# Kernel optimization log

Hardware: AMD Instinct MI355X
Metric: run time of the kernel (lower is better)

Reference implementation:

```python
import jax, jax.numpy as jnp
import numpy as np

N, H, E, R, Q = 10000, 128, 160000, 32, 1
CUT = 5.0  # cutoff_upper, cutoff_lower = 0


def setup_inputs() -> dict:
    key = jax.random.key(0)
    ks = jax.random.split(key, 16)

    def w(k, shape, fan_in):
        return jax.random.normal(k, shape, jnp.float32) / np.sqrt(fan_in).astype(np.float32)

    return dict(
        X=jax.random.normal(ks[0], (N, H, 3, 3), jnp.float32),
        charges=jax.random.normal(ks[1], (N, Q), jnp.float32),
        edge_attr=jax.random.normal(ks[2], (E, R), jnp.float32),
        edge_weight=jax.random.uniform(ks[3], (E,), jnp.float32, 0.0, CUT),
        W1=w(ks[4], (H, R + 2 * Q), R + 2 * Q), b1=jnp.zeros((H,), jnp.float32),
        W2=w(ks[5], (2 * H, H), H), b2=jnp.zeros((2 * H,), jnp.float32),
        W3=w(ks[6], (3 * H, 2 * H), 2 * H), b3=jnp.zeros((3 * H,), jnp.float32),
        Wt0=w(ks[7], (H, H), H), Wt1=w(ks[8], (H, H), H), Wt2=w(ks[9], (H, H), H),
        Wt3=w(ks[10], (H, H), H), Wt4=w(ks[11], (H, H), H), Wt5=w(ks[12], (H, H), H),
        edge_index=jax.random.randint(ks[13], (2, E), 0, N),
    )


def tensor_norm(T):
    return jnp.sum(T * T, axis=(-2, -1))  # [N, H]


def decompose(T):
    # I: mean of diagonal (scalar per channel); A: skew part; S: traceless symmetric part
    I = jnp.trace(T, axis1=-2, axis2=-1) / 3.0  # [N, H]
    Tt = jnp.swapaxes(T, -2, -1)
    A = 0.5 * (T - Tt)
    S = 0.5 * (T + Tt) - I[..., None, None] * jnp.eye(3, dtype=T.dtype)
    return I, A, S


def chlin(T, W):
    # channel-mixing linear on [N, H, 3, 3]; torch Linear: y_o = sum_h x_h W[o, h]
    return jnp.einsum('nhij,oh->noij', T, W)


def vec_to_skew(v):
    # v: [N, H, 3] -> skew-symmetric [N, H, 3, 3]
    z = jnp.zeros_like(v[..., 0])
    return jnp.stack([
        jnp.stack([z, -v[..., 2], v[..., 1]], -1),
        jnp.stack([v[..., 2], z, -v[..., 0]], -1),
        jnp.stack([-v[..., 1], v[..., 0], z], -1),
    ], -2)


def skew_to_vec(A):
    return jnp.stack([A[..., 2, 1], A[..., 0, 2], A[..., 1, 0]], -1)


def reference(X, charges, edge_attr, edge_weight, W1, b1, W2, b2, W3, b3,
              Wt0, Wt1, Wt2, Wt3, Wt4, Wt5, edge_index):
    eye = jnp.eye(3, dtype=X.dtype)
    src, dst = edge_index[0], edge_index[1]
    n = X.shape[0]

    # cosine cutoff (cutoff_lower = 0)
    C = 0.5 * (jnp.cos(jnp.pi * edge_weight / CUT) + 1.0) * (edge_weight < CUT)

    # edge scalar MLP
    x = jnp.concatenate([edge_attr, charges[src], charges[dst]], axis=-1)
    x = jax.nn.silu(x @ W1.T + b1)
    x = jax.nn.silu(x @ W2.T + b2)
    x = jax.nn.silu(x @ W3.T + b3)
    x = (x * C[:, None]).reshape(-1, 3, H)  # [E, 3, H]

    X = X / (tensor_norm(X) + 1.0)[..., None, None]
    I, A, S = decompose(X)
    I = I @ Wt0.T
    A = chlin(A, Wt1)
    S = chlin(S, Wt2)
    Y = A + S + I[..., None, None] * eye

    # message passing: gather at dst, weight by edge scalars, scatter-add to src
    Im = jax.ops.segment_sum(x[:, 0, :] * I[dst], src, num_segments=n)
    Am = jax.ops.segment_sum(x[:, 1, :, None] * skew_to_vec(A)[dst], src, num_segments=n)
    Sm = jax.ops.segment_sum(x[:, 2, :, None, None] * S[dst], src, num_segments=n)
    msg = vec_to_skew(Am) + Sm + Im[..., None, None] * eye

    # O(3) equivariance: symmetrized product
    M = jnp.matmul(msg, Y) + jnp.matmul(Y, msg)
    I, A, S = decompose(M)

    _X = A + S + I[..., None, None] * eye
    normp1 = tensor_norm(_X) + 1.0
    I = I / normp1
    A = A / normp1[..., None, None]
    S = S / normp1[..., None, None]
    I = I @ Wt3.T
    A = chlin(A, Wt4)
    S = chlin(S, Wt5)
    dX = A + S + I[..., None, None] * eye
    return X + dX + jnp.matmul(dX, dX)
```

## Files before the change

### kernel.cpp

```cpp
#include <hip/hip_runtime.h>

#define NN  10000
#define HD  128
#define EE  160000
#define RD  32
#define NH  (NN * HD)

typedef __attribute__((ext_vector_type(8))) short short8_t;
typedef __attribute__((ext_vector_type(4))) float f32x4_t;
typedef __attribute__((ext_vector_type(4))) int   int4_t;

__device__ __forceinline__ float silu_f(float z) {
    return z * __builtin_amdgcn_rcpf(1.0f + __expf(-z));
}
__device__ __forceinline__ short f2b(float v) {
    unsigned u = __float_as_uint(v);
    unsigned r = (u + 0x7FFFu + ((u >> 16) & 1u)) >> 16;
    return (short)r;
}
__device__ __forceinline__ float b2f(short s) {
    return __uint_as_float(((unsigned)(unsigned short)s) << 16);
}
__device__ __forceinline__ unsigned cvt_pk(float a, float b) {
    unsigned r;
    asm("v_cvt_pk_bf16_f32 %0, %1, %2" : "=v"(r) : "v"(a), "v"(b));
    return r;
}

__global__ __launch_bounds__(256) void k_wconv(
    const float* __restrict__ W1, const float* __restrict__ W2,
    const float* __restrict__ W3,
    const float* __restrict__ Wt0, const float* __restrict__ Wt1,
    const float* __restrict__ Wt2, const float* __restrict__ Wt3,
    const float* __restrict__ Wt4, const float* __restrict__ Wt5,
    short* __restrict__ W1b, short* __restrict__ W2b, short* __restrict__ W3b,
    short* __restrict__ WtPh, short* __restrict__ WtPl,
    short* __restrict__ WtFh, short* __restrict__ WtFl)
{
    const int i = blockIdx.x * 256 + threadIdx.x;
    if (i < 8192) {
        const int j = i & 7, lane = (i >> 3) & 63;
        const int kb = (i >> 9) & 1, ct = i >> 10;
        const int n = ct * 16 + (lane & 15);
        const int k = kb * 32 + (lane >> 4) * 8 + j;
        W1b[i] = (k < 34) ? f2b(W1[n * 34 + k]) : (short)0;
        return;
    }
    int j2 = i - 8192;
    if (j2 < 32768) {
        const int j = j2 & 7, lane = (j2 >> 3) & 63;
        const int kb = (j2 >> 9) & 3, ct = j2 >> 11;
        const int n = ct * 16 + (lane & 15);
        const int k = kb * 32 + (lane >> 4) * 8 + j;
        W2b[j2] = f2b(W2[n * 128 + k]);
        return;
    }
    j2 -= 32768;
    if (j2 < 98304) {
        const int j = j2 & 7, lane = (j2 >> 3) & 63;
        const int kb = (j2 >> 9) & 7, ct = j2 >> 12;
        const int n = ct * 16 + (lane & 15);
        const int k = kb * 32 + (lane >> 4) * 8 + j;
        W3b[j2] = f2b(W3[n * 256 + k]);
        return;
    }
    j2 -= 98304;
    if (j2 < 6 * 16384) {
        const int m = j2 >> 14, idx = j2 & 16383;
        const float* src = (m == 0) ? Wt0 : (m == 1) ? Wt1 : (m == 2) ? Wt2
                         : (m == 3) ? Wt3 : (m == 4) ? Wt4 : Wt5;
        const float w = src[idx];
        const short hi = f2b(w);
        const short lo = f2b(w - b2f(hi));
        if (m < 3) { WtPh[m * 16384 + idx] = hi; WtPl[m * 16384 + idx] = lo; }
        else       { WtFh[(m - 3) * 16384 + idx] = hi; WtFl[(m - 3) * 16384 + idx] = lo; }
    }
}

template <bool FIN, bool WB>
__global__ __launch_bounds__(512, 4) void k_mix(
    const float* __restrict__ X,
    const float* __restrict__ Yin, const float* __restrict__ MSGin,
    const short* __restrict__ Wh,  const short* __restrict__ Wl,
    float* __restrict__ outp, short* __restrict__ ybf)
{
    extern __shared__ __align__(16) char smem[];
    short* sBh = (short*)smem;
    short* sBl = sBh + 144 * 128;
    float* sC  = (float*)smem;

    const int tid = threadIdx.x;
    const int n0  = blockIdx.x * 16;

#pragma unroll 2
    for (int i = 0; i < 4; i++) {
        const int p  = i * 512 + tid;
        const int nl = p >> 7, h = p & 127;
        float dec[9];
        if constexpr (!FIN) {
            const float* t = X + ((size_t)((n0 + nl) * HD + h)) * 9;
            float T[9];
#pragma unroll
            for (int q = 0; q < 9; q++) T[q] = t[q];
            float nrm = 0.f;
#pragma unroll
            for (int q = 0; q < 9; q++) nrm = fmaf(T[q], T[q], nrm);
            const float inv = 1.0f / (nrm + 1.0f);
#pragma unroll
            for (int q = 0; q < 9; q++) T[q] *= inv;
            const float I = (T[0] + T[4] + T[8]) * (1.0f / 3.0f);
            dec[0] = I;
            dec[1] = 0.5f * (T[7] - T[5]);
            dec[2] = 0.5f * (T[2] - T[6]);
            dec[3] = 0.5f * (T[3] - T[1]);
            dec[4] = T[0] - I;
            dec[5] = 0.5f * (T[1] + T[3]);
            dec[6] = 0.5f * (T[2] + T[6]);
            dec[7] = T[4] - I;
            dec[8] = 0.5f * (T[5] + T[7]);
        } else {
            const int basep = (n0 + nl) * HD + h;
            float yv[9], mv[9];
#pragma unroll
            for (int c = 0; c < 9; c++) {
                yv[c] = Yin[(size_t)c * NH + basep];
                mv[c] = MSGin[(size_t)c * NH + basep];
            }
            float Yt[9], G[9];
            {
                const float I = yv[0], a0 = yv[1], a1 = yv[2], a2 = yv[3];
                const float s00 = yv[4], s01 = yv[5], s02 = yv[6], s11 = yv[7], s12 = yv[8];
                const float s22 = -s00 - s11;
                Yt[0] = I + s00; Yt[1] = s01 - a2; Yt[2] = s02 + a1;
                Yt[3] = s01 + a2; Yt[4] = I + s11; Yt[5] = s12 - a0;
                Yt[6] = s02 - a1; Yt[7] = s12 + a0; Yt[8] = I + s22;
            }
            {
                const float I = mv[0], a0 = mv[1], a1 = mv[2], a2 = mv[3];
                const float s00 = mv[4], s01 = mv[5], s02 = mv[6], s11 = mv[7], s12 = mv[8];
                const float s22 = -s00 - s11;
                G[0] = I + s00; G[1] = s01 - a2; G[2] = s02 + a1;
                G[3] = s01 + a2; G[4] = I + s11; G[5] = s12 - a0;
                G[6] = s02 - a1; G[7] = s12 + a0; G[8] = I + s22;
            }
            float M[9];
#pragma unroll
            for (int r = 0; r < 3; r++)
#pragma unroll
                for (int cc = 0; cc < 3; cc++) {
                    float a = 0.f;
#pragma unroll
                    for (int k = 0; k < 3; k++)
                        a += G[r * 3 + k] * Yt[k * 3 + cc]
                           + Yt[r * 3 + k] * G[k * 3 + cc];
                    M[r * 3 + cc] = a;
                }
            const float I2 = (M[0] + M[4] + M[8]) * (1.0f / 3.0f);
            const float a0 = 0.5f * (M[7] - M[5]);
            const float a1 = 0.5f * (M[2] - M[6]);
            const float a2 = 0.5f * (M[3] - M[1]);
            const float s00 = M[0] - I2, s11 = M[4] - I2;
            const float s01 = 0.5f * (M[1] + M[3]);
            const float s02 = 0.5f * (M[2] + M[6]);
            const float s12 = 0.5f * (M[5] + M[7]);
            const float s22 = -s00 - s11;
            const float nrm = 2.f * (a0 * a0 + a1 * a1 + a2 * a2)
                            + (s00 * s00 + s11 * s11 + s22 * s22)
                            + 2.f * (s01 * s01 + s02 * s02 + s12 * s12)
                            + 3.f * I2 * I2;
            const float inv = 1.0f / (nrm + 1.0f);
            dec[0] = I2 * inv;  dec[1] = a0 * inv;  dec[2] = a1 * inv;
            dec[3] = a2 * inv;  dec[4] = s00 * inv; dec[5] = s01 * inv;
            dec[6] = s02 * inv; dec[7] = s11 * inv; dec[8] = s12 * inv;
        }
        const int sw = (nl & 7) << 3;
        const int hx = h ^ sw;
#pragma unroll
        for (int c = 0; c < 9; c++) {
            const float v  = dec[c];
            const short hi = f2b(v);
            const short lo = f2b(v - b2f(hi));
            const int idx = (c * 16 + nl) * 128 + hx;
            sBh[idx] = hi;
            sBl[idx] = lo;
        }
    }
    __syncthreads();

    const int lane = tid & 63, wid = tid >> 6;
    const int l15 = lane & 15, g = lane >> 4;
    f32x4_t acc[9];
#pragma unroll
    for (int c = 0; c < 9; c++) acc[c] = {0.f, 0.f, 0.f, 0.f};

    const int bsw = (l15 & 7) << 3;
    const int o   = wid * 16 + l15;
#pragma unroll
    for (int k = 0; k < 4; k++) {
        const int k0  = k * 32 + g * 8;
        const int ksw = k0 ^ bsw;
#pragma unroll
        for (int w = 0; w < 3; w++) {
            const size_t aoff = (size_t)w * 16384 + (size_t)o * 128 + k0;
            const short8_t Ah = *(const short8_t*)(Wh + aoff);
            const short8_t Al = *(const short8_t*)(Wl + aoff);
            const int ct0 = (w == 0) ? 0 : (w == 1 ? 1 : 4);
            const int ctn = (w == 0) ? 1 : (w == 1 ? 3 : 5);
            for (int cc = 0; cc < ctn; cc++) {
                const int ct = ct0 + cc;
                const int boff = (ct * 16 + l15) * 128 + ksw;
                const short8_t Bh = *(const short8_t*)&sBh[boff];
                const short8_t Bl = *(const short8_t*)&sBl[boff];
                acc[ct] = __builtin_amdgcn_mfma_f32_16x16x32_bf16(Al, Bh, acc[ct], 0, 0, 0);
                acc[ct] = __builtin_amdgcn_mfma_f32_16x16x32_bf16(Ah, Bl, acc[ct], 0, 0, 0);
                acc[ct] = __builtin_amdgcn_mfma_f32_16x16x32_bf16(Ah, Bh, acc[ct], 0, 0, 0);
            }
        }
    }
    __syncthreads();

    const int csw = (l15 & 7) << 2;
    {
        const int o0 = wid * 16 + g * 4;
#pragma unroll
        for (int ct = 0; ct < 9; ct++)
            *(f32x4_t*)&sC[(ct * 16 + l15) * 128 + (o0 ^ csw)] = acc[ct];
    }
    __syncthreads();

    if constexpr (!FIN) {
        for (int i = tid; i < 144 * 32; i += 512) {
            const int row = i >> 5, q = i & 31;
            const int c = row >> 4, nl = row & 15;
            const int sw = (nl & 7) << 2;
            const f32x4_t v = *(const f32x4_t*)&sC[row * 128 + ((q * 4) ^ sw)];
            const size_t oo = (size_t)c * NH + (size_t)(n0 + nl) * HD + q * 4;
            *(f32x4_t*)&outp[oo] = v;
            if constexpr (WB) {
                uint2 u;
                u.x = cvt_pk(v[0], v[1]);
                u.y = cvt_pk(v[2], v[3]);
                *(uint2*)&ybf[oo] = u;
            }
        }
    } else {
#pragma unroll 2
        for (int i = 0; i < 4; i++) {
            const int p  = i * 512 + tid;
            const int nl = p >> 7, oo = p & 127;
            const int sw = (nl & 7) << 2;
            const int ox = oo ^ sw;
            float a9[9];
#pragma unroll
            for (int c = 0; c < 9; c++) a9[c] = sC[(c * 16 + nl) * 128 + ox];
            float D[9];
            {
                const float I = a9[0], a0 = a9[1], a1 = a9[2], a2 = a9[3];
                const float s00 = a9[4], s01 = a9[5], s02 = a9[6];
                const float s11 = a9[7], s12 = a9[8];
                const float s22 = -s00 - s11;
                D[0] = I + s00; D[1] = s01 - a2; D[2] = s02 + a1;
                D[3] = s01 + a2; D[4] = I + s11; D[5] = s12 - a0;
                D[6] = s02 - a1; D[7] = s12 + a0; D[8] = I + s22;
            }
            const size_t xbase = ((size_t)((n0 + nl) * HD + oo)) * 9;
            float T[9];
#pragma unroll
            for (int q = 0; q < 9; q++) T[q] = X[xbase + q];
            float nrm = 0.f;
#pragma unroll
            for (int q = 0; q < 9; q++) nrm = fmaf(T[q], T[q], nrm);
            const float inv = 1.0f / (nrm + 1.0f);
            float* op = outp + xbase;
#pragma unroll
            for (int r = 0; r < 3; r++)
#pragma unroll
                for (int cc = 0; cc < 3; cc++) {
                    float dd2 = 0.f;
#pragma unroll
                    for (int k = 0; k < 3; k++)
                        dd2 = fmaf(D[r * 3 + k], D[k * 3 + cc], dd2);
                    op[r * 3 + cc] = T[r * 3 + cc] * inv + D[r * 3 + cc] + dd2;
                }
        }
    }
}

__global__ __launch_bounds__(256) void k_count(const int* __restrict__ EI,
                                               int* __restrict__ cnt)
{
    const int e = blockIdx.x * 256 + threadIdx.x;
    atomicAdd(&cnt[EI[e]], 1);
}

__global__ __launch_bounds__(256) void k_scan(const int* __restrict__ cnt,
                                              int* __restrict__ offs,
                                              int* __restrict__ cur)
{
    __shared__ int part[256];
    const int tid = threadIdx.x;
    const int per = (NN + 255) / 256;
    int s = 0;
    for (int i = 0; i < per; i++) {
        const int idx = tid * per + i;
        if (idx < NN) s += cnt[idx];
    }
    part[tid] = s;
    __syncthreads();
    if (tid == 0) {
        int r = 0;
        for (int i = 0; i < 256; i++) { const int t = part[i]; part[i] = r; r += t; }
        offs[NN] = r;
    }
    __syncthreads();
    int run = part[tid];
    for (int i = 0; i < per; i++) {
        const int idx = tid * per + i;
        if (idx < NN) {
            offs[idx] = run;
            cur[idx]  = run;
            run += cnt[idx];
        }
    }
}

__global__ __launch_bounds__(256) void k_fill(const int* __restrict__ EI,
                                              int* __restrict__ cur,
                                              int* __restrict__ EIDS,
                                              int* __restrict__ DSTS)
{
    const int e = blockIdx.x * 256 + threadIdx.x;
    const int s = EI[e];
    const int pos = atomicAdd(&cur[s], 1);
    EIDS[pos] = e;
    DSTS[pos] = EI[EE + e];
}

__global__ __launch_bounds__(512, 4) void k_edge_mfma(
    const float* __restrict__ EA, const float* __restrict__ CH,
    const float* __restrict__ EW, const int*   __restrict__ EI,
    const short* __restrict__ W1b, const float* __restrict__ b1,
    const short* __restrict__ W2b, const float* __restrict__ b2,
    const short* __restrict__ W3b, const float* __restrict__ b3,
    short* __restrict__ XC)
{
    __shared__ __align__(16) short sH2[64 * 256];
    __shared__ __align__(16) short sH1[64 * 128];
    __shared__ float sCut[64];

    short* sIn = sH2;
    const int tid = threadIdx.x;
    const int e0  = blockIdx.x * 64;

    {
        int4_t z = {0, 0, 0, 0};
        ((int4_t*)sIn)[tid] = z;
    }
    __syncthreads();
    {
        const float4 v = ((const float4*)(EA + (size_t)e0 * RD))[tid];
        const int e = tid >> 3;
        const int k = (tid & 7) * 4;
        short4 sv;
        sv.x = f2b(v.x); sv.y = f2b(v.y); sv.z = f2b(v.z); sv.w = f2b(v.w);
        *(short4*)&sIn[e * 64 + (k ^ ((e & 7) << 3))] = sv;
        if (tid < 64) {
            const int ee = tid;
            const int s = EI[e0 + ee];
            const int d = EI[EE + e0 + ee];
            const int sw = (ee & 7) << 3;
            sIn[ee * 64 + (32 ^ sw)] = f2b(CH[s]);
            sIn[ee * 64 + (33 ^ sw)] = f2b(CH[d]);
            const float w = EW[e0 + ee];
            sCut[ee] = (w < 5.0f)
                     ? 0.5f * (__cosf(0.62831853071795864769f * w) + 1.0f) : 0.0f;
        }
    }
    __syncthreads();

    const int lane = tid & 63;
    const int wid  = tid >> 6;
    const int l15  = lane & 15;
    const int g    = lane >> 4;
    const int fsw  = l15 << 3;

    {
        short8_t E1[4][2];
#pragma unroll
        for (int at = 0; at < 4; at++) {
            const int row = at * 16 + l15;
            const int x = (row & 7) << 3;
            E1[at][0] = *(const short8_t*)&sIn[row * 64 + ((g * 8) ^ x)];
            E1[at][1] = *(const short8_t*)&sIn[row * 64 + ((32 + g * 8) ^ x)];
        }
        const int ct = wid;
        const float4 b4 = *(const float4*)&b1[ct * 16 + g * 4];
        const short8_t av0 = *(const short8_t*)(W1b + (size_t)((ct * 2 + 0) * 64 + lane) * 8);
        const short8_t av1 = *(const short8_t*)(W1b + (size_t)((ct * 2 + 1) * 64 + lane) * 8);
        const int fcol = ct * 16 + g * 4;
#pragma unroll
        for (int at = 0; at < 4; at++) {
            f32x4_t acc = {b4.x, b4.y, b4.z, b4.w};
            acc = __builtin_amdgcn_mfma_f32_16x16x32_bf16(av0, E1[at][0], acc, 0, 0, 0);
            acc = __builtin_amdgcn_mfma_f32_16x16x32_bf16(av1, E1[at][1], acc, 0, 0, 0);
            const int edge = at * 16 + l15;
            uint2 u;
            u.x = cvt_pk(silu_f(acc[0]), silu_f(acc[1]));
            u.y = cvt_pk(silu_f(acc[2]), silu_f(acc[3]));
            *(uint2*)&sH1[edge * 128 + (fcol ^ fsw)] = u;
        }
    }
    __syncthreads();

    {
        short8_t E2[4][4];
#pragma unroll
        for (int at = 0; at < 4; at++) {
            const int row = at * 16 + l15;
            const int x = (row & 15) << 3;
#pragma unroll
            for (int kb = 0; kb < 4; kb++)
                E2[at][kb] = *(const short8_t*)&sH1[row * 128 + ((kb * 32 + g * 8) ^ x)];
        }
#pragma unroll
        for (int c = 0; c < 2; c++) {
            const int ct = c * 8 + wid;
            const float4 b4 = *(const float4*)&b2[ct * 16 + g * 4];
            const int fcol = ct * 16 + g * 4;
            f32x4_t acc[4];
#pragma unroll
            for (int at = 0; at < 4; at++) acc[at] = {b4.x, b4.y, b4.z, b4.w};
#pragma unroll
            for (int kb = 0; kb < 4; kb++) {
                const short8_t av = *(const short8_t*)(W2b + (size_t)((ct * 4 + kb) * 64 + lane) * 8);
#pragma unroll
                for (int at = 0; at < 4; at++)
                    acc[at] = __builtin_amdgcn_mfma_f32_16x16x32_bf16(av, E2[at][kb], acc[at], 0, 0, 0);
            }
#pragma unroll
            for (int at = 0; at < 4; at++) {
                const int edge = at * 16 + l15;
                uint2 u;
                u.x = cvt_pk(silu_f(acc[at][0]), silu_f(acc[at][1]));
                u.y = cvt_pk(silu_f(acc[at][2]), silu_f(acc[at][3]));
                *(uint2*)&sH2[edge * 256 + (fcol ^ fsw)] = u;
            }
        }
    }
    __syncthreads();

    {
        short8_t E3[4][8];
#pragma unroll
        for (int at = 0; at < 4; at++) {
            const int row = at * 16 + l15;
            const int x = (row & 15) << 3;
#pragma unroll
            for (int kb = 0; kb < 8; kb++)
                E3[at][kb] = *(const short8_t*)&sH2[row * 256 + ((kb * 32 + g * 8) ^ x)];
        }
        float cut[4];
#pragma unroll
        for (int at = 0; at < 4; at++) cut[at] = sCut[at * 16 + l15];
        for (int c = 0; c < 3; c++) {
            const int ct = c * 8 + wid;
            const float4 b4 = *(const float4*)&b3[ct * 16 + g * 4];
            const int fcol = ct * 16 + g * 4;
            f32x4_t acc[4];
#pragma unroll
            for (int at = 0; at < 4; at++) acc[at] = {b4.x, b4.y, b4.z, b4.w};
#pragma unroll
            for (int kb = 0; kb < 8; kb++) {
                const short8_t av = *(const short8_t*)(W3b + (size_t)((ct * 8 + kb) * 64 + lane) * 8);
#pragma unroll
                for (int at = 0; at < 4; at++)
                    acc[at] = __builtin_amdgcn_mfma_f32_16x16x32_bf16(av, E3[at][kb], acc[at], 0, 0, 0);
            }
#pragma unroll
            for (int at = 0; at < 4; at++) {
                const int edge = at * 16 + l15;
                const float cv = cut[at];
                uint2 u;
                u.x = cvt_pk(silu_f(acc[at][0]) * cv, silu_f(acc[at][1]) * cv);
                u.y = cvt_pk(silu_f(acc[at][2]) * cv, silu_f(acc[at][3]) * cv);
                *(uint2*)&XC[(size_t)(e0 + edge) * 384 + fcol] = u;
            }
        }
    }
}

__global__ __launch_bounds__(256) void k_edge_atomic(
    const float* __restrict__ EA, const float* __restrict__ CH,
    const float* __restrict__ EW, const int*   __restrict__ EI,
    const float* __restrict__ W1, const float* __restrict__ b1,
    const float* __restrict__ W2, const float* __restrict__ b2,
    const float* __restrict__ W3, const float* __restrict__ b3,
    const float* __restrict__ Y,  float* __restrict__ MSG)
{
    __shared__ __align__(16) float sInf[32 * 35];
    __shared__ __align__(16) float sH1f[32 * 132];
    __shared__ __align__(16) float sH2f[32 * 260];
    __shared__ __align__(16) float sXcf[32 * 132];
    __shared__ float sCc[32];
    __shared__ int   sS[32], sD[32];

    const int e0  = blockIdx.x * 32;
    const int tid = threadIdx.x;

    {
        const float4 v = ((const float4*)(EA + (size_t)e0 * RD))[tid];
        const int e = tid >> 3;
        const int k = (tid & 7) * 4;
        float* p = sInf + e * 35 + k;
        p[0] = v.x; p[1] = v.y; p[2] = v.z; p[3] = v.w;
    }
    if (tid < 32) {
        const int e = tid;
        const int s = EI[e0 + e];
        const int d = EI[EE + e0 + e];
        sS[e] = s; sD[e] = d;
        sInf[e * 35 + 32] = CH[s];
        sInf[e * 35 + 33] = CH[d];
        const float w = EW[e0 + e];
        sCc[e] = (w < 5.0f) ? 0.5f * (__cosf(0.62831853071795864769f * w) + 1.0f)
                            : 0.0f;
    }
    __syncthreads();

    const int e  = tid & 31;
    const int og = tid >> 5;

    {
        float acc[16];
#pragma unroll
        for (int j = 0; j < 16; j++) acc[j] = b1[og * 16 + j];
        for (int k = 0; k < 34; k++) {
            const float v = sInf[e * 35 + k];
#pragma unroll
            for (int j = 0; j < 16; j++)
                acc[j] = fmaf(v, W1[(og * 16 + j) * 34 + k], acc[j]);
        }
#pragma unroll
        for (int j = 0; j < 16; j++)
            sH1f[e * 132 + og * 16 + j] = silu_f(acc[j]);
    }
    __syncthreads();

    {
        float acc[32];
#pragma unroll
        for (int j = 0; j < 32; j++) acc[j] = b2[og * 32 + j];
        for (int hq = 0; hq < 32; hq++) {
            const float4 v = *(const float4*)&sH1f[e * 132 + hq * 4];
#pragma unroll
            for (int j = 0; j < 32; j++) {
                const float4 w =
                    *(const float4*)&W2[(size_t)(og * 32 + j) * 128 + hq * 4];
                acc[j] = fmaf(v.x, w.x, fmaf(v.y, w.y,
                         fmaf(v.z, w.z, fmaf(v.w, w.w, acc[j]))));
            }
        }
#pragma unroll
        for (int j = 0; j < 32; j++)
            sH2f[e * 260 + og * 32 + j] = silu_f(acc[j]);
    }
    __syncthreads();

    for (int c = 0; c < 3; c++) {
        {
            float acc[16];
#pragma unroll
            for (int j = 0; j < 16; j++) acc[j] = b3[c * 128 + og * 16 + j];
            for (int hq = 0; hq < 64; hq++) {
                const float4 v = *(const float4*)&sH2f[e * 260 + hq * 4];
#pragma unroll
                for (int j = 0; j < 16; j++) {
                    const float4 w = *(const float4*)
                        &W3[(size_t)(c * 128 + og * 16 + j) * 256 + hq * 4];
                    acc[j] = fmaf(v.x, w.x, fmaf(v.y, w.y,
                             fmaf(v.z, w.z, fmaf(v.w, w.w, acc[j]))));
                }
            }
            const float cc = sCc[e];
#pragma unroll
            for (int j = 0; j < 16; j++)
                sXcf[e * 132 + og * 16 + j] = silu_f(acc[j]) * cc;
        }
        __syncthreads();
        {
            const int h  = tid & 127;
            const int eh = tid >> 7;
#pragma unroll 4
            for (int i = 0; i < 16; i++) {
                const int ee = (eh << 4) | i;
                const int s = sS[ee], d = sD[ee];
                const float xv = sXcf[ee * 132 + h];
                const int sb = s * HD + h, db = d * HD + h;
                if (c == 0) {
                    atomicAdd(&MSG[0 * (size_t)NH + sb], xv * Y[0 * (size_t)NH + db]);
                } else if (c == 1) {
#pragma unroll
                    for (int cc2 = 1; cc2 < 4; cc2++)
                        atomicAdd(&MSG[(size_t)cc2 * NH + sb],
                                  xv * Y[(size_t)cc2 * NH + db]);
                } else {
#pragma unroll
                    for (int cc2 = 4; cc2 < 9; cc2++)
                        atomicAdd(&MSG[(size_t)cc2 * NH + sb],
                                  xv * Y[(size_t)cc2 * NH + db]);
                }
            }
        }
        __syncthreads();
    }
}

__device__ __forceinline__ float ldy(const float* p) { return *p; }
__device__ __forceinline__ float ldy(const short* p) { return b2f(*p); }

template <typename YT>
__global__ __launch_bounds__(256) void k_gather(
    const short* __restrict__ XC, const YT* __restrict__ Y,
    const int* __restrict__ offs, const int* __restrict__ EIDS,
    const int* __restrict__ DSTS, float* __restrict__ MSG)
{
    const int tid = threadIdx.x;
    const int nl  = tid >> 7, h = tid & 127;
    const int n   = blockIdx.x * 2 + nl;
    const int beg = offs[n], end = offs[n + 1];

    float m[9];
#pragma unroll
    for (int c = 0; c < 9; c++) m[c] = 0.f;

    for (int p = beg; p < end; ++p) {
        const int eid = EIDS[p];
        const int dst = DSTS[p];
        const size_t xb = (size_t)eid * 384;
        const float x0 = b2f(XC[xb + h]);
        const float x1 = b2f(XC[xb + 128 + h]);
        const float x2 = b2f(XC[xb + 256 + h]);
        const int yb = dst * HD + h;
        m[0] = fmaf(x0, ldy(Y + 0 * (size_t)NH + yb), m[0]);
        m[1] = fmaf(x1, ldy(Y + 1 * (size_t)NH + yb), m[1]);
        m[2] = fmaf(x1, ldy(Y + 2 * (size_t)NH + yb), m[2]);
        m[3] = fmaf(x1, ldy(Y + 3 * (size_t)NH + yb), m[3]);
        m[4] = fmaf(x2, ldy(Y + 4 * (size_t)NH + yb), m[4]);
        m[5] = fmaf(x2, ldy(Y + 5 * (size_t)NH + yb), m[5]);
        m[6] = fmaf(x2, ldy(Y + 6 * (size_t)NH + yb), m[6]);
        m[7] = fmaf(x2, ldy(Y + 7 * (size_t)NH + yb), m[7]);
        m[8] = fmaf(x2, ldy(Y + 8 * (size_t)NH + yb), m[8]);
    }
    const int base = n * HD + h;
#pragma unroll
    for (int c = 0; c < 9; c++) MSG[(size_t)c * NH + base] = m[c];
}

static inline size_t align_up(size_t v, size_t a) { return (v + a - 1) & ~(a - 1); }

extern "C" void kernel_launch(void* const* d_in, const int* in_sizes, int n_in,
                              void* d_out, int out_size, void* d_ws, size_t ws_size,
                              hipStream_t stream)
{
    const float* X   = (const float*)d_in[0];
    const float* CH  = (const float*)d_in[1];
    const float* EA  = (const float*)d_in[2];
    const float* EW  = (const float*)d_in[3];
    const float* W1  = (const float*)d_in[4];
    const float* b1  = (const float*)d_in[5];
    const float* W2  = (const float*)d_in[6];
    const float* b2  = (const float*)d_in[7];
    const float* W3  = (const float*)d_in[8];
    const float* b3  = (const float*)d_in[9];
    const float* Wt0 = (const float*)d_in[10];
    const float* Wt1 = (const float*)d_in[11];
    const float* Wt2 = (const float*)d_in[12];
    const float* Wt3 = (const float*)d_in[13];
    const float* Wt4 = (const float*)d_in[14];
    const float* Wt5 = (const float*)d_in[15];
    const int*   EI  = (const int*)d_in[16];
    float* out = (float*)d_out;

    size_t off = 0;
    float* Y    = (float*)((char*)d_ws + off); off = align_up(off + (size_t)9 * NH * 4, 64);
    float* MSG  = (float*)((char*)d_ws + off); off = align_up(off + (size_t)9 * NH * 4, 64);
    int*   cnt  = (int*)((char*)d_ws + off);   off = align_up(off + (size_t)NN * 4, 64);
    int*   cur  = (int*)((char*)d_ws + off);   off = align_up(off + (size_t)NN * 4, 64);
    int*   offs = (int*)((char*)d_ws + off);   off = align_up(off + (size_t)(NN + 1) * 4, 64);
    int*   EIDS = (int*)((char*)d_ws + off);   off = align_up(off + (size_t)EE * 4, 64);
    int*   DSTS = (int*)((char*)d_ws + off);   off = align_up(off + (size_t)EE * 4, 64);
    short* W1b  = (short*)((char*)d_ws + off); off = align_up(off + (size_t)8192 * 2, 64);
    short* W2b  = (short*)((char*)d_ws + off); off = align_up(off + (size_t)32768 * 2, 64);
    short* W3b  = (short*)((char*)d_ws + off); off = align_up(off + (size_t)98304 * 2, 64);
    short* WtPh = (short*)((char*)d_ws + off); off = align_up(off + (size_t)3 * 16384 * 2, 64);
    short* WtPl = (short*)((char*)d_ws + off); off = align_up(off + (size_t)3 * 16384 * 2, 64);
    short* WtFh = (short*)((char*)d_ws + off); off = align_up(off + (size_t)3 * 16384 * 2, 64);
    short* WtFl = (short*)((char*)d_ws + off); off = align_up(off + (size_t)3 * 16384 * 2, 64);
    short* XC   = (short*)((char*)d_ws + off); off = align_up(off + (size_t)EE * 384 * 2, 64);
    const size_t need_plain = off;
    short* Ybf  = (short*)((char*)d_ws + off); off = align_up(off + (size_t)9 * NH * 2, 64);
    const size_t need_ybf = off;

    k_wconv<<<928, 256, 0, stream>>>(W1, W2, W3, Wt0, Wt1, Wt2, Wt3, Wt4, Wt5,
                                     W1b, W2b, W3b, WtPh, WtPl, WtFh, WtFl);

    if (ws_size >= need_plain) {
        const bool use_ybf = (ws_size >= need_ybf);
        if (use_ybf)
            k_mix<false, true><<<NN / 16, 512, 73728, stream>>>(
                X, Y, Y, WtPh, WtPl, Y, Ybf);
        else
            k_mix<false, false><<<NN / 16, 512, 73728, stream>>>(
                X, Y, Y, WtPh, WtPl, Y, nullptr);

        hipMemsetAsync(cnt, 0, (size_t)NN * sizeof(int), stream);
        k_count<<<EE / 256, 256, 0, stream>>>(EI, cnt);
        k_scan<<<1, 256, 0, stream>>>(cnt, offs, cur);
        k_fill<<<EE / 256, 256, 0, stream>>>(EI, cur, EIDS, DSTS);
        k_edge_mfma<<<EE / 64, 512, 0, stream>>>(EA, CH, EW, EI,
                                                 W1b, b1, W2b, b2, W3b, b3, XC);
        if (use_ybf)
            k_gather<short><<<NN / 2, 256, 0, stream>>>(XC, Ybf, offs, EIDS, DSTS, MSG);
        else
            k_gather<float><<<NN / 2, 256, 0, stream>>>(XC, Y, offs, EIDS, DSTS, MSG);
    } else {
        k_mix<false, false><<<NN / 16, 512, 73728, stream>>>(
            X, Y, Y, WtPh, WtPl, Y, nullptr);
        hipMemsetAsync(MSG, 0, (size_t)9 * NH * sizeof(float), stream);
        k_edge_atomic<<<EE / 32, 256, 0, stream>>>(EA, CH, EW, EI,
                                                   W1, b1, W2, b2, W3, b3, Y, MSG);
    }

    k_mix<true, false><<<NN / 16, 512, 73728, stream>>>(X, Y, MSG, WtFh, WtFl, out, nullptr);
}
```

Baseline: 306.3 us.

## Write edge features in sorted order and store messages as bf16

The edge MLP kernel now writes each edge's 384-wide feature row directly at its position in the CSR order sorted by source, using a permutation computed in the fill kernel. The gather can then read XC contiguously and no longer needs the EIDS indirection. The aggregated message tensor is also stored in bf16 instead of fp32, halving its write and read traffic into the final mix kernel. The cost is a scattered write pattern in the edge kernel and lower precision on the messages; the fallback paths for a smaller workspace are simplified.

```diff
diff --git a/kernel.cpp b/kernel.cpp
--- a/kernel.cpp
+++ b/kernel.cpp
@@ -77,10 +77,13 @@
     }
 }
 
-template <bool FIN, bool WB>
+__device__ __forceinline__ float ldy(const float* p) { return *p; }
+__device__ __forceinline__ float ldy(const short* p) { return b2f(*p); }
+
+template <bool FIN, bool WB, typename MT>
 __global__ __launch_bounds__(512, 4) void k_mix(
     const float* __restrict__ X,
-    const float* __restrict__ Yin, const float* __restrict__ MSGin,
+    const float* __restrict__ Yin, const MT* __restrict__ MSGin,
     const short* __restrict__ Wh,  const short* __restrict__ Wl,
     float* __restrict__ outp, short* __restrict__ ybf)
 {
@@ -124,7 +127,7 @@
 #pragma unroll
             for (int c = 0; c < 9; c++) {
                 yv[c] = Yin[(size_t)c * NH + basep];
-                mv[c] = MSGin[(size_t)c * NH + basep];
+                mv[c] = ldy(MSGin + (size_t)c * NH + basep);
             }
             float Yt[9], G[9];
             {
@@ -326,19 +329,20 @@
 
 __global__ __launch_bounds__(256) void k_fill(const int* __restrict__ EI,
                                               int* __restrict__ cur,
-                                              int* __restrict__ EIDS,
+                                              int* __restrict__ PERM,
                                               int* __restrict__ DSTS)
 {
     const int e = blockIdx.x * 256 + threadIdx.x;
     const int s = EI[e];
     const int pos = atomicAdd(&cur[s], 1);
-    EIDS[pos] = e;
+    PERM[e] = pos;
     DSTS[pos] = EI[EE + e];
 }
 
 __global__ __launch_bounds__(512, 4) void k_edge_mfma(
     const float* __restrict__ EA, const float* __restrict__ CH,
     const float* __restrict__ EW, const int*   __restrict__ EI,
+    const int*   __restrict__ PERM,
     const short* __restrict__ W1b, const float* __restrict__ b1,
     const short* __restrict__ W2b, const float* __restrict__ b2,
     const short* __restrict__ W3b, const float* __restrict__ b3,
@@ -347,6 +351,7 @@
     __shared__ __align__(16) short sH2[64 * 256];
     __shared__ __align__(16) short sH1[64 * 128];
     __shared__ float sCut[64];
+    __shared__ int   sPerm[64];
 
     short* sIn = sH2;
     const int tid = threadIdx.x;
@@ -374,6 +379,7 @@
             const float w = EW[e0 + ee];
             sCut[ee] = (w < 5.0f)
                      ? 0.5f * (__cosf(0.62831853071795864769f * w) + 1.0f) : 0.0f;
+            sPerm[ee] = PERM[e0 + ee];
         }
     }
     __syncthreads();
@@ -460,8 +466,12 @@
                 E3[at][kb] = *(const short8_t*)&sH2[row * 256 + ((kb * 32 + g * 8) ^ x)];
         }
         float cut[4];
-#pragma unroll
-        for (int at = 0; at < 4; at++) cut[at] = sCut[at * 16 + l15];
+        int   prm[4];
+#pragma unroll
+        for (int at = 0; at < 4; at++) {
+            cut[at] = sCut[at * 16 + l15];
+            prm[at] = sPerm[at * 16 + l15];
+        }
         for (int c = 0; c < 3; c++) {
             const int ct = c * 8 + wid;
             const float4 b4 = *(const float4*)&b3[ct * 16 + g * 4];
@@ -478,12 +488,11 @@
             }
 #pragma unroll
             for (int at = 0; at < 4; at++) {
-                const int edge = at * 16 + l15;
                 const float cv = cut[at];
                 uint2 u;
                 u.x = cvt_pk(silu_f(acc[at][0]) * cv, silu_f(acc[at][1]) * cv);
                 u.y = cvt_pk(silu_f(acc[at][2]) * cv, silu_f(acc[at][3]) * cv);
-                *(uint2*)&XC[(size_t)(e0 + edge) * 384 + fcol] = u;
+                *(uint2*)&XC[(size_t)prm[at] * 384 + fcol] = u;
             }
         }
     }
@@ -615,14 +624,10 @@
     }
 }
 
-__device__ __forceinline__ float ldy(const float* p) { return *p; }
-__device__ __forceinline__ float ldy(const short* p) { return b2f(*p); }
-
-template <typename YT>
 __global__ __launch_bounds__(256) void k_gather(
-    const short* __restrict__ XC, const YT* __restrict__ Y,
-    const int* __restrict__ offs, const int* __restrict__ EIDS,
-    const int* __restrict__ DSTS, float* __restrict__ MSG)
+    const short* __restrict__ XC, const short* __restrict__ Y,
+    const int* __restrict__ offs, const int* __restrict__ DSTS,
+    short* __restrict__ MSGb)
 {
     const int tid = threadIdx.x;
     const int nl  = tid >> 7, h = tid & 127;
@@ -634,26 +639,25 @@
     for (int c = 0; c < 9; c++) m[c] = 0.f;
 
     for (int p = beg; p < end; ++p) {
-        const int eid = EIDS[p];
         const int dst = DSTS[p];
-        const size_t xb = (size_t)eid * 384;
+        const size_t xb = (size_t)p * 384;
         const float x0 = b2f(XC[xb + h]);
         const float x1 = b2f(XC[xb + 128 + h]);
         const float x2 = b2f(XC[xb + 256 + h]);
         const int yb = dst * HD + h;
-        m[0] = fmaf(x0, ldy(Y + 0 * (size_t)NH + yb), m[0]);
-        m[1] = fmaf(x1, ldy(Y + 1 * (size_t)NH + yb), m[1]);
-        m[2] = fmaf(x1, ldy(Y + 2 * (size_t)NH + yb), m[2]);
-        m[3] = fmaf(x1, ldy(Y + 3 * (size_t)NH + yb), m[3]);
-        m[4] = fmaf(x2, ldy(Y + 4 * (size_t)NH + yb), m[4]);
-        m[5] = fmaf(x2, ldy(Y + 5 * (size_t)NH + yb), m[5]);
-        m[6] = fmaf(x2, ldy(Y + 6 * (size_t)NH + yb), m[6]);
-        m[7] = fmaf(x2, ldy(Y + 7 * (size_t)NH + yb), m[7]);
-        m[8] = fmaf(x2, ldy(Y + 8 * (size_t)NH + yb), m[8]);
+        m[0] = fmaf(x0, b2f(Y[0 * (size_t)NH + yb]), m[0]);
+        m[1] = fmaf(x1, b2f(Y[1 * (size_t)NH + yb]), m[1]);
+        m[2] = fmaf(x1, b2f(Y[2 * (size_t)NH + yb]), m[2]);
+        m[3] = fmaf(x1, b2f(Y[3 * (size_t)NH + yb]), m[3]);
+        m[4] = fmaf(x2, b2f(Y[4 * (size_t)NH + yb]), m[4]);
+        m[5] = fmaf(x2, b2f(Y[5 * (size_t)NH + yb]), m[5]);
+        m[6] = fmaf(x2, b2f(Y[6 * (size_t)NH + yb]), m[6]);
+        m[7] = fmaf(x2, b2f(Y[7 * (size_t)NH + yb]), m[7]);
+        m[8] = fmaf(x2, b2f(Y[8 * (size_t)NH + yb]), m[8]);
     }
     const int base = n * HD + h;
 #pragma unroll
-    for (int c = 0; c < 9; c++) MSG[(size_t)c * NH + base] = m[c];
+    for (int c = 0; c < 9; c++) MSGb[(size_t)c * NH + base] = f2b(m[c]);
 }
 
 static inline size_t align_up(size_t v, size_t a) { return (v + a - 1) & ~(a - 1); }
@@ -684,10 +688,11 @@
     size_t off = 0;
     float* Y    = (float*)((char*)d_ws + off); off = align_up(off + (size_t)9 * NH * 4, 64);
     float* MSG  = (float*)((char*)d_ws + off); off = align_up(off + (size_t)9 * NH * 4, 64);
+    short* MSGb = (short*)MSG;
     int*   cnt  = (int*)((char*)d_ws + off);   off = align_up(off + (size_t)NN * 4, 64);
     int*   cur  = (int*)((char*)d_ws + off);   off = align_up(off + (size_t)NN * 4, 64);
     int*   offs = (int*)((char*)d_ws + off);   off = align_up(off + (size_t)(NN + 1) * 4, 64);
-    int*   EIDS = (int*)((char*)d_ws + off);   off = align_up(off + (size_t)EE * 4, 64);
+    int*   PERM = (int*)((char*)d_ws + off);   off = align_up(off + (size_t)EE * 4, 64);
     int*   DSTS = (int*)((char*)d_ws + off);   off = align_up(off + (size_t)EE * 4, 64);
     short* W1b  = (short*)((char*)d_ws + off); off = align_up(off + (size_t)8192 * 2, 64);
     short* W2b  = (short*)((char*)d_ws + off); off = align_up(off + (size_t)32768 * 2, 64);
@@ -697,39 +702,33 @@
     short* WtFh = (short*)((char*)d_ws + off); off = align_up(off + (size_t)3 * 16384 * 2, 64);
     short* WtFl = (short*)((char*)d_ws + off); off = align_up(off + (size_t)3 * 16384 * 2, 64);
     short* XC   = (short*)((char*)d_ws + off); off = align_up(off + (size_t)EE * 384 * 2, 64);
-    const size_t need_plain = off;
     short* Ybf  = (short*)((char*)d_ws + off); off = align_up(off + (size_t)9 * NH * 2, 64);
-    const size_t need_ybf = off;
+    const size_t need_fast = off;
 
     k_wconv<<<928, 256, 0, stream>>>(W1, W2, W3, Wt0, Wt1, Wt2, Wt3, Wt4, Wt5,
                                      W1b, W2b, W3b, WtPh, WtPl, WtFh, WtFl);
 
-    if (ws_size >= need_plain) {
-        const bool use_ybf = (ws_size >= need_ybf);
-        if (use_ybf)
-            k_mix<false, true><<<NN / 16, 512, 73728, stream>>>(
-                X, Y, Y, WtPh, WtPl, Y, Ybf);
-        else
-            k_mix<false, false><<<NN / 16, 512, 73728, stream>>>(
-                X, Y, Y, WtPh, WtPl, Y, nullptr);
+    if (ws_size >= need_fast) {
+        k_mix<false, true, float><<<NN / 16, 512, 73728, stream>>>(
+            X, Y, Y, WtPh, WtPl, Y, Ybf);
 
         hipMemsetAsync(cnt, 0, (size_t)NN * sizeof(int), stream);
         k_count<<<EE / 256, 256, 0, stream>>>(EI, cnt);
         k_scan<<<1, 256, 0, stream>>>(cnt, offs, cur);
-        k_fill<<<EE / 256, 256, 0, stream>>>(EI, cur, EIDS, DSTS);
-        k_edge_mfma<<<EE / 64, 512, 0, stream>>>(EA, CH, EW, EI,
+        k_fill<<<EE / 256, 256, 0, stream>>>(EI, cur, PERM, DSTS);
+        k_edge_mfma<<<EE / 64, 512, 0, stream>>>(EA, CH, EW, EI, PERM,
                                                  W1b, b1, W2b, b2, W3b, b3, XC);
-        if (use_ybf)
-            k_gather<short><<<NN / 2, 256, 0, stream>>>(XC, Ybf, offs, EIDS, DSTS, MSG);
-        else
-            k_gather<float><<<NN / 2, 256, 0, stream>>>(XC, Y, offs, EIDS, DSTS, MSG);
+        k_gather<<<NN / 2, 256, 0, stream>>>(XC, Ybf, offs, DSTS, MSGb);
+
+        k_mix<true, false, short><<<NN / 16, 512, 73728, stream>>>(
+            X, Y, MSGb, WtFh, WtFl, out, nullptr);
     } else {
-        k_mix<false, false><<<NN / 16, 512, 73728, stream>>>(
+        k_mix<false, false, float><<<NN / 16, 512, 73728, stream>>>(
             X, Y, Y, WtPh, WtPl, Y, nullptr);
         hipMemsetAsync(MSG, 0, (size_t)9 * NH * sizeof(float), stream);
         k_edge_atomic<<<EE / 32, 256, 0, stream>>>(EA, CH, EW, EI,
                                                    W1, b1, W2, b2, W3, b3, Y, MSG);
-    }
-
-    k_mix<true, false><<<NN / 16, 512, 73728, stream>>>(X, Y, MSG, WtFh, WtFl, out, nullptr);
-}
+        k_mix<true, false, float><<<NN / 16, 512, 73728, stream>>>(
+            X, Y, MSG, WtFh, WtFl, out, nullptr);
+    }
+}
```

Result: no change. 305.4 us (-0.3%).
